# Kernel tuning notes

Hardware: AMD Instinct MI355X
Metric: run time of the kernel (lower is better)

Reference implementation:

```python
import jax, jax.numpy as jnp
import numpy as np

V = 32          # num_variables
T = 48          # num_time_bins
D = 512         # d_model
H = 8           # num_heads
HD = D // H     # head_dim = 64
OD = 16         # observation_dim
B = 4


def setup_inputs() -> dict:
    key = jax.random.key(0)
    ks = jax.random.split(key, 20)
    s = 0.02
    inp = {
        'h': jax.random.normal(ks[0], (B, T, V, D), jnp.float32),
        'observation_state': jax.random.normal(ks[1], (B, T, V, 2), jnp.float32),
        'Wq': jax.random.normal(ks[2], (D, D), jnp.float32) * s,
        'bq': jnp.zeros((D,), jnp.float32),
        'Wk': jax.random.normal(ks[3], (D, D), jnp.float32) * s,
        'bk': jnp.zeros((D,), jnp.float32),
        'Wv': jax.random.normal(ks[4], (D, D), jnp.float32) * s,
        'bv': jnp.zeros((D,), jnp.float32),
        'Wo': jax.random.normal(ks[5], (D, D), jnp.float32) * s,
        'bo': jnp.zeros((D,), jnp.float32),
        'Woq': jax.random.normal(ks[6], (2, H * OD), jnp.float32) * 0.5,
        'boq': jnp.zeros((H * OD,), jnp.float32),
        'Wok': jax.random.normal(ks[7], (2, H * OD), jnp.float32) * 0.5,
        'bok': jnp.zeros((H * OD,), jnp.float32),
        'variable_bias': jax.random.normal(ks[8], (H, V, V), jnp.float32) * 0.01,
        'relative_time_bias': jax.random.normal(ks[9], (H, 2 * T - 1), jnp.float32) * 0.01,
    }
    return inp


def reference(h, observation_state, Wq, bq, Wk, bk, Wv, bv, Wo, bo,
              Woq, boq, Wok, bok, variable_bias, relative_time_bias):
    N = T * V
    scale = 1.0 / np.sqrt(HD)
    obs_scale = 1.0 / np.sqrt(OD)

    # static index buffers (constants)
    flat_var_ids = jnp.tile(jnp.arange(V), T)                       # [N]
    flat_time_ids = jnp.repeat(jnp.arange(T), V)                    # [N]
    rel_index = flat_time_ids[:, None] - flat_time_ids[None, :] + (T - 1)  # [N,N]

    fh = h.reshape(B, N, D)
    fo = observation_state.reshape(B, N, 2)

    def heads(x, nh, hd):
        return x.reshape(B, N, nh, hd).transpose(0, 2, 1, 3)  # [B,H,N,hd]

    q = heads(fh @ Wq + bq, H, HD)
    k = heads(fh @ Wk + bk, H, HD)
    v = heads(fh @ Wv + bv, H, HD)
    oq = heads(fo @ Woq + boq, H, OD)
    ok = heads(fo @ Wok + bok, H, OD)

    content = jnp.einsum('bhnd,bhmd->bhnm', q, k) * scale
    obs = jnp.einsum('bhnd,bhmd->bhnm', oq, ok) * obs_scale
    var_scores = variable_bias[:, flat_var_ids[:, None], flat_var_ids[None, :]]  # [H,N,N]
    time_scores = relative_time_bias[:, rel_index]                                # [H,N,N]

    scores = content + obs + var_scores[None] + time_scores[None]
    attn = jax.nn.softmax(scores, axis=-1)  # dropout off (inference)
    out = jnp.einsum('bhnm,bhmd->bhnd', attn, v)
    out = out.transpose(0, 2, 1, 3).reshape(B, N, D)
    out = out @ Wo + bo
    return out.reshape(B, T, V, D)
```

## Files before the change

kernel.cpp:

```cpp
#include <hip/hip_runtime.h>
#include <math.h>

typedef __bf16 bf16x8 __attribute__((ext_vector_type(8)));
typedef float f32x4 __attribute__((ext_vector_type(4)));
typedef short short4v __attribute__((ext_vector_type(4)));

#define NB 4
#define NT 48
#define NV 32
#define ND 512
#define NH 8
#define NN 1536
#define NBN 6144
#define L2E 1.44269504f

#define GLOAD_LDS(g, l) \
    __builtin_amdgcn_global_load_lds( \
        (const __attribute__((address_space(1))) void*)(g), \
        (__attribute__((address_space(3))) void*)(l), 16, 0, 0)

__global__ __launch_bounds__(256) void prep(
    const float* __restrict__ h, const float* __restrict__ obs,
    const float* __restrict__ Wq, const float* __restrict__ Wk,
    const float* __restrict__ Wv, const float* __restrict__ Wo,
    const float* __restrict__ bq, const float* __restrict__ bk,
    const float* __restrict__ bv,
    const float* __restrict__ Wok, const float* __restrict__ bok,
    __bf16* __restrict__ h_bf, __bf16* __restrict__ WcatT,
    __bf16* __restrict__ WoT, float* __restrict__ biascat,
    __bf16* __restrict__ kx)
{
    __shared__ float ts[64][68];
    const int tid = threadIdx.x;
    const int bx = blockIdx.x;
    if (bx < 1536) {
        int t = bx * 256 + tid;
        const float4* src = (const float4*)h + (size_t)t * 2;
        float4 a = src[0], b = src[1];
        __bf16 r[8] = {(__bf16)a.x, (__bf16)a.y, (__bf16)a.z, (__bf16)a.w,
                       (__bf16)b.x, (__bf16)b.y, (__bf16)b.z, (__bf16)b.w};
        *(uint4*)(h_bf + (size_t)t * 8) = *(uint4*)r;
    } else if (bx < 1792) {
        int bw = bx - 1536;
        const int p = bw >> 6, tile = bw & 63;
        const int k0 = (tile >> 3) * 64, c0 = (tile & 7) * 64;
        const float* W = (p == 0) ? Wq : (p == 1) ? Wk : (p == 2) ? Wv : Wo;
        const float scale = (p == 0) ? 0.125f * L2E : 1.0f;
        #pragma unroll
        for (int i = 0; i < 4; i++) {
            int r = (tid >> 4) + i * 16;
            float4 v = *(const float4*)(W + (size_t)(k0 + r) * 512 + c0 + (tid & 15) * 4);
            *(float4*)&ts[r][(tid & 15) * 4] = v;
        }
        __syncthreads();
        __bf16 tmp[16];
        #pragma unroll
        for (int j = 0; j < 16; j++)
            tmp[j] = (__bf16)(ts[(tid & 3) * 16 + j][tid >> 2] * scale);
        int crow = c0 + (tid >> 2);
        __bf16* dst = (p < 3)
            ? WcatT + ((size_t)(p * 512 + crow)) * 512 + k0 + (tid & 3) * 16
            : WoT   + ((size_t)crow) * 512 + k0 + (tid & 3) * 16;
        *(uint4*)dst = *(uint4*)tmp;
        *(uint4*)(dst + 8) = *(uint4*)(tmp + 8);
        if (p < 3 && k0 == 0 && tid < 64) {
            const float* bb = (p == 0) ? bq : (p == 1) ? bk : bv;
            biascat[p * 512 + c0 + tid] = bb[c0 + tid] * scale;
        }
    } else {
        int t = (bx - 1792) * 256 + tid;
        int row = t >> 1, half = t & 1;
        int bh = row / NN, n = row - bh * NN;
        int mt = n >> 6, wv = (n >> 4) & 3, l16k = n & 15;
        __bf16* dst = kx + (((size_t)(bh * 24 + mt) * 4 + wv) * 3 + 2) * 512
                         + (half * 2) * 128 + l16k * 8;
        if (half == 0) {
            int hh = bh & 7;
            int b = bh >> 3;
            size_t bn = (size_t)b * NN + n;
            float o0 = obs[bn * 2], o1 = obs[bn * 2 + 1];
            int f = hh * 16;
            __bf16 tmp[16];
            #pragma unroll
            for (int j = 0; j < 16; j++)
                tmp[j] = (__bf16)(o0 * Wok[f + j] + o1 * Wok[128 + f + j] + bok[f + j]);
            *(uint4*)dst         = *(uint4*)tmp;
            *(uint4*)(dst + 128) = *(uint4*)(tmp + 8);
        } else {
            uint4 z = {0, 0, 0, 0};
            *(uint4*)dst         = z;
            *(uint4*)(dst + 128) = z;
        }
    }
}

template<int TM, bool BF16OUT>
__global__ __launch_bounds__(256) void gemm_mfma(
    const __bf16* __restrict__ A, const __bf16* __restrict__ Bt,
    const float* __restrict__ bias, float* __restrict__ Cf,
    __bf16* __restrict__ qarr, __bf16* __restrict__ kx,
    __bf16* __restrict__ vt)
{
    constexpr int MT = TM / 32;
    __shared__ __align__(16) char smem[34816];
    char* const As0 = smem;
    char* const As1 = smem + TM * 64;
    char* const Bs0 = smem + TM * 128;
    char* const Bs1 = smem + TM * 128 + 8192;
    const int tid = threadIdx.x;
    const int w = tid >> 6, lane = tid & 63;
    const int quad = lane >> 4, l16 = lane & 15;
    const int wm = w >> 1, wn = w & 1;
    const int n0 = blockIdx.x * 128, m0 = blockIdx.y * TM;

    const int sm = tid >> 2;
    const int sk = ((tid & 3) ^ ((sm >> 1) & 3)) * 8;
    const __bf16* aptr = A  + (size_t)(m0 + sm) * 512 + sk;
    const __bf16* bptr = Bt + (size_t)(n0 + sm) * 512 + sk;

    f32x4 zero4 = {0.f, 0.f, 0.f, 0.f};
    f32x4 acc[MT][4];
    #pragma unroll
    for (int i = 0; i < MT; i++)
        #pragma unroll
        for (int j = 0; j < 4; j++) acc[i][j] = zero4;

    auto STAGE = [&](char* dA, char* dB, int kt) {
        GLOAD_LDS(aptr + kt, dA + tid * 16);
        if (TM == 128) GLOAD_LDS(aptr + 64 * 512 + kt, dA + 4096 + tid * 16);
        GLOAD_LDS(bptr + kt, dB + tid * 16);
        GLOAD_LDS(bptr + 64 * 512 + kt, dB + 4096 + tid * 16);
    };
    auto COMPUTE = [&](const char* Asb, const char* Bsb) {
        bf16x8 af[MT], bfr[4];
        #pragma unroll
        for (int mt = 0; mt < MT; mt++) {
            int rr = wm * (TM / 2) + mt * 16 + l16;
            af[mt] = *(const bf16x8*)(Asb + rr * 64 + (quad ^ ((rr >> 1) & 3)) * 16);
        }
        #pragma unroll
        for (int nt = 0; nt < 4; nt++) {
            int rr = wn * 64 + nt * 16 + l16;
            bfr[nt] = *(const bf16x8*)(Bsb + rr * 64 + (quad ^ ((rr >> 1) & 3)) * 16);
        }
        #pragma unroll
        for (int mt = 0; mt < MT; mt++)
            #pragma unroll
            for (int nt = 0; nt < 4; nt++)
                acc[mt][nt] = __builtin_amdgcn_mfma_f32_16x16x32_bf16(
                    af[mt], bfr[nt], acc[mt][nt], 0, 0, 0);
    };

    STAGE(As0, Bs0, 0);
    asm volatile("s_waitcnt vmcnt(0)" ::: "memory");
    __builtin_amdgcn_s_barrier();
    for (int kt = 0; kt < 512; kt += 64) {
        STAGE(As1, Bs1, kt + 32);
        COMPUTE(As0, Bs0);
        asm volatile("s_waitcnt vmcnt(0)" ::: "memory");
        __builtin_amdgcn_s_barrier();
        if (kt + 64 < 512) STAGE(As0, Bs0, kt + 64);
        COMPUTE(As1, Bs1);
        asm volatile("s_waitcnt vmcnt(0)" ::: "memory");
        __builtin_amdgcn_s_barrier();
    }

    __syncthreads();
    if (BF16OUT) {
        if (n0 >= 1024) {
            __bf16* CsT = (__bf16*)smem;
            #pragma unroll
            for (int nt = 0; nt < 4; nt++) {
                int cl = wn * 64 + nt * 16 + l16;
                float bia = bias[n0 + cl];
                #pragma unroll
                for (int mt = 0; mt < MT; mt++) {
                    int rl0 = wm * (TM / 2) + mt * 16 + quad * 4;
                    __bf16 pk[4];
                    #pragma unroll
                    for (int r = 0; r < 4; r++)
                        pk[r] = (__bf16)(acc[mt][nt][r] + bia);
                    *(uint2*)&CsT[cl * 136 + rl0] = *(uint2*)pk;
                }
            }
            __syncthreads();
            int cl = tid >> 1, half = tid & 1;
            int f0 = (n0 + cl) & 511;
            int hh = f0 >> 6, d = f0 & 63;
            int dt = d >> 4, l16v = d & 15;
            int bidx = m0 / NN, nm = m0 - bidx * NN;
            int bh = bidx * 8 + hh;
            int mtv = (nm >> 6) + half;
            #pragma unroll
            for (int j = 0; j < 8; j++) {
                uint4 v = *(uint4*)&CsT[cl * 136 + half * 64 + j * 8];
                __bf16* pp = (__bf16*)&v;
                size_t fo = (((size_t)(bh * 24 + mtv) * 4 + (j >> 1)) * 4 + dt) * 256;
                int q0 = (j & 1) * 2;
                *(uint2*)(vt + fo + q0 * 64 + l16v * 4)       = *(uint2*)&pp[0];
                *(uint2*)(vt + fo + (q0 + 1) * 64 + l16v * 4) = *(uint2*)&pp[4];
            }
        } else {
            __bf16* Cs = (__bf16*)smem;
            #pragma unroll
            for (int mt = 0; mt < MT; mt++)
                #pragma unroll
                for (int nt = 0; nt < 4; nt++) {
                    int cl = wn * 64 + nt * 16 + l16;
                    float bia = bias[n0 + cl];
                    #pragma unroll
                    for (int r = 0; r < 4; r++) {
                        int rl = wm * (TM / 2) + mt * 16 + quad * 4 + r;
                        Cs[rl * 132 + cl] = (__bf16)(acc[mt][nt][r] + bia);
                    }
                }
            __syncthreads();
            int rl = tid >> 1, hb = tid & 1;
            int grow = m0 + rl;
            int col0 = n0 + hb * 64;
            int p = col0 >> 9, f0 = col0 & 511, hh = f0 >> 6;
            int bidx = grow / NN, n = grow - bidx * NN;
            if (p == 0) {
                __bf16* dst = qarr + (size_t)grow * 512 + f0;
                #pragma unroll
                for (int j = 0; j < 8; j++) {
                    uint2 lo = *(uint2*)&Cs[rl * 132 + hb * 64 + j * 8];
                    uint2 hi = *(uint2*)&Cs[rl * 132 + hb * 64 + j * 8 + 4];
                    uint4 v = {lo.x, lo.y, hi.x, hi.y};
                    *(uint4*)(dst + j * 8) = v;
                }
            } else {
                int mtk = n >> 6, wv = (n >> 4) & 3, l16k = n & 15;
                size_t fb = ((size_t)((bidx * 8 + hh) * 24 + mtk) * 4 + wv) * 1536;
                #pragma unroll
                for (int j = 0; j < 8; j++) {
                    uint2 lo = *(uint2*)&Cs[rl * 132 + hb * 64 + j * 8];
                    uint2 hi = *(uint2*)&Cs[rl * 132 + hb * 64 + j * 8 + 4];
                    uint4 v = {lo.x, lo.y, hi.x, hi.y};
                    *(uint4*)(kx + fb + (j >> 2) * 512 + (j & 3) * 128 + l16k * 8) = v;
                }
            }
        }
    } else {
        float* Csf = (float*)smem;
        #pragma unroll
        for (int mt = 0; mt < MT; mt++)
            #pragma unroll
            for (int nt = 0; nt < 4; nt++) {
                int cl = wn * 64 + nt * 16 + l16;
                float bia = bias[n0 + cl];
                #pragma unroll
                for (int r = 0; r < 4; r++) {
                    int rl = wm * (TM / 2) + mt * 16 + quad * 4 + r;
                    Csf[rl * 132 + cl] = acc[mt][nt][r] + bia;
                }
            }
        __syncthreads();
        int rl = tid >> 2, q4 = tid & 3;
        float* dst = Cf + (size_t)(m0 + rl) * 512 + n0 + q4 * 32;
        #pragma unroll
        for (int j = 0; j < 8; j++) {
            uint4 v = *(uint4*)&Csf[rl * 132 + q4 * 32 + j * 4];
            *(uint4*)(dst + j * 4) = v;
        }
    }
}

__global__ __launch_bounds__(256) void attn_mfma(
    const __bf16* __restrict__ qarr, const __bf16* __restrict__ kx,
    const __bf16* __restrict__ vt, const float* __restrict__ obs,
    const float* __restrict__ Woq, const float* __restrict__ boq,
    const float* __restrict__ varb, const float* __restrict__ rtb,
    __bf16* __restrict__ aout)
{
    __shared__ float Or[64][68];
    __shared__ float lps[4][64];
    __shared__ float2 rts2[96];

    const int tid = threadIdx.x;
    const int w = tid >> 6, lane = tid & 63;
    const int quad = lane >> 4, l16 = lane & 15;
    const int bh = blockIdx.x, qt = blockIdx.y;
    const int b = bh >> 3, h = bh & 7;
    const int n0 = qt * 64;

    if (tid < 95) {
        float a = rtb[h * 95 + tid] * L2E;
        float c = (tid < 94) ? rtb[h * 95 + tid + 1] * L2E : 0.f;
        rts2[tid].x = a;
        rts2[tid].y = c;
    }

    const __bf16* kwb = kx + ((size_t)bh * 24 * 4 + w) * 1536 + lane * 8;
    const __bf16* vwb = vt + ((size_t)bh * 24 * 4 + w) * 1024 + lane * 4;

    bf16x8 qf[4][3];
    #pragma unroll
    for (int nt = 0; nt < 4; nt++) {
        const size_t qrow = (size_t)(b * NN + n0 + nt * 16 + l16);
        qf[nt][0] = *(const bf16x8*)(qarr + qrow * 512 + h * 64 + quad * 8);
        qf[nt][1] = *(const bf16x8*)(qarr + qrow * 512 + h * 64 + 32 + quad * 8);
        uint4 a2u = {0u, 0u, 0u, 0u};
        if (quad < 2) {
            float o0 = obs[qrow * 2], o1 = obs[qrow * 2 + 1];
            int f = h * 16 + quad * 8;
            const float scq = 0.25f * L2E;
            __bf16 tmp[8];
            #pragma unroll
            for (int j = 0; j < 8; j++)
                tmp[j] = (__bf16)(scq * (o0 * Woq[f + j] + o1 * Woq[128 + f + j]
                                         + boq[f + j]));
            a2u = *(uint4*)tmp;
        }
        qf[nt][2] = *(bf16x8*)&a2u;
    }

    const float* vbp = varb + h * 1024 + (w & 1) * 16 + quad * 4;
    f32x4 vvA = *(const f32x4*)(vbp + l16 * 32);
    f32x4 vvB = *(const f32x4*)(vbp + (16 + l16) * 32);
    vvA *= L2E; vvB *= L2E;

    const int rbase = 2 * qt - (w >> 1) + 47;

    f32x4 zero4 = {0.f, 0.f, 0.f, 0.f};
    f32x4 o_p[4][4];
    #pragma unroll
    for (int i = 0; i < 4; i++)
        #pragma unroll
        for (int j = 0; j < 4; j++) o_p[i][j] = zero4;
    float lp_s[4] = {0.f, 0.f, 0.f, 0.f};

    bf16x8 kc[3]; short4v vc[4];
    #pragma unroll
    for (int ks = 0; ks < 3; ks++) kc[ks] = *(const bf16x8*)(kwb + ks * 512);
    #pragma unroll
    for (int dt = 0; dt < 4; dt++) vc[dt] = *(const short4v*)(vwb + dt * 256);

    __syncthreads();

    for (int mt = 0; mt < 24; mt++) {
        bf16x8 kn[3]; short4v vn[4];
        if (mt + 1 < 24) {
            const __bf16* kp = kwb + (size_t)(mt + 1) * 6144;
            const __bf16* vp = vwb + (size_t)(mt + 1) * 4096;
            #pragma unroll
            for (int ks = 0; ks < 3; ks++) kn[ks] = *(const bf16x8*)(kp + ks * 512);
            #pragma unroll
            for (int dt = 0; dt < 4; dt++) vn[dt] = *(const short4v*)(vp + dt * 256);
        }

        f32x4 sc[4];
        __builtin_amdgcn_s_setprio(1);
        #pragma unroll
        for (int nt = 0; nt < 4; nt++) {
            f32x4 d = zero4;
            #pragma unroll
            for (int ks = 0; ks < 3; ks++)
                d = __builtin_amdgcn_mfma_f32_16x16x32_bf16(kc[ks], qf[nt][ks], d, 0, 0, 0);
            sc[nt] = d;
        }
        __builtin_amdgcn_s_setprio(0);

        float2 tb = rts2[rbase - 2 * mt];
        short4v pf[4];
        #pragma unroll
        for (int nt = 0; nt < 4; nt++) {
            float tbx = (nt < 2) ? tb.x : tb.y;
            const f32x4& vv = (nt & 1) ? vvB : vvA;
            union { __bf16 e[4]; short4v s; } pk;
            #pragma unroll
            for (int r = 0; r < 4; r++) {
                float p = exp2f(sc[nt][r] + vv[r] + tbx);
                lp_s[nt] += p;
                pk.e[r] = (__bf16)p;
            }
            pf[nt] = pk.s;
        }

        __builtin_amdgcn_s_setprio(1);
        #pragma unroll
        for (int nt = 0; nt < 4; nt++)
            #pragma unroll
            for (int dt = 0; dt < 4; dt++)
                o_p[dt][nt] = __builtin_amdgcn_mfma_f32_16x16x16bf16_1k(
                    vc[dt], pf[nt], o_p[dt][nt], 0, 0, 0);
        __builtin_amdgcn_s_setprio(0);

        if (mt + 1 < 24) {
            #pragma unroll
            for (int ks = 0; ks < 3; ks++) kc[ks] = kn[ks];
            #pragma unroll
            for (int dt = 0; dt < 4; dt++) vc[dt] = vn[dt];
        }
    }

    #pragma unroll
    for (int nt = 0; nt < 4; nt++) {
        lp_s[nt] += __shfl_xor(lp_s[nt], 16);
        lp_s[nt] += __shfl_xor(lp_s[nt], 32);
    }
    if (quad == 0) {
        #pragma unroll
        for (int nt = 0; nt < 4; nt++) lps[w][nt * 16 + l16] = lp_s[nt];
    }

    #pragma unroll
    for (int ws = 0; ws < 4; ws++) {
        if (w == ws) {
            #pragma unroll
            for (int dt = 0; dt < 4; dt++)
                #pragma unroll
                for (int nt = 0; nt < 4; nt++) {
                    float* dst = &Or[nt * 16 + l16][dt * 16 + quad * 4];
                    if (ws == 0) *(f32x4*)dst = o_p[dt][nt];
                    else {
                        f32x4 t = *(f32x4*)dst;
                        *(f32x4*)dst = t + o_p[dt][nt];
                    }
                }
        }
        __syncthreads();
    }

    int n = tid >> 2, dq = tid & 3;
    float linv = 1.0f / (lps[0][n] + lps[1][n] + lps[2][n] + lps[3][n]);
    __bf16 ov[16];
    #pragma unroll
    for (int jj = 0; jj < 4; jj++) {
        f32x4 t = *(f32x4*)&Or[n][dq * 16 + jj * 4];
        ov[jj * 4 + 0] = (__bf16)(t[0] * linv);
        ov[jj * 4 + 1] = (__bf16)(t[1] * linv);
        ov[jj * 4 + 2] = (__bf16)(t[2] * linv);
        ov[jj * 4 + 3] = (__bf16)(t[3] * linv);
    }
    size_t abase = ((size_t)(b * NN) + n0 + n) * 512 + h * 64 + dq * 16;
    *(uint4*)(aout + abase)     = *(uint4*)&ov[0];
    *(uint4*)(aout + abase + 8) = *(uint4*)&ov[8];
}

extern "C" void kernel_launch(void* const* d_in, const int* in_sizes, int n_in,
                              void* d_out, int out_size, void* d_ws, size_t ws_size,
                              hipStream_t stream)
{
    const float* h_   = (const float*)d_in[0];
    const float* obs  = (const float*)d_in[1];
    const float* Wq   = (const float*)d_in[2];
    const float* bq   = (const float*)d_in[3];
    const float* Wk   = (const float*)d_in[4];
    const float* bk   = (const float*)d_in[5];
    const float* Wv   = (const float*)d_in[6];
    const float* bv   = (const float*)d_in[7];
    const float* Wo   = (const float*)d_in[8];
    const float* bo   = (const float*)d_in[9];
    const float* Woq  = (const float*)d_in[10];
    const float* boq  = (const float*)d_in[11];
    const float* Wok  = (const float*)d_in[12];
    const float* bok  = (const float*)d_in[13];
    const float* varb = (const float*)d_in[14];
    const float* rtb  = (const float*)d_in[15];
    float* out = (float*)d_out;

    char* ws = (char*)d_ws;
    __bf16* h_bf    = (__bf16*)ws;                 ws += (size_t)NBN * 512 * 2;
    __bf16* qarr    = (__bf16*)ws;                 ws += (size_t)NBN * 512 * 2;
    __bf16* vt      = (__bf16*)ws;                 ws += (size_t)NBN * 512 * 2;
    __bf16* kx      = (__bf16*)ws;                 ws += ((size_t)32 * NN * 96 + 64) * 2;
    __bf16* attnout = (__bf16*)ws;                 ws += (size_t)NBN * 512 * 2;
    __bf16* WcatT   = (__bf16*)ws;                 ws += (size_t)1536 * 512 * 2;
    __bf16* WoT     = (__bf16*)ws;                 ws += (size_t)512 * 512 * 2;
    float*  biascat = (float*)ws;                  ws += 1536 * 4;

    prep<<<dim3(2176), dim3(256), 0, stream>>>(
        h_, obs, Wq, Wk, Wv, Wo, bq, bk, bv, Wok, bok,
        h_bf, WcatT, WoT, biascat, kx);
    gemm_mfma<128, true><<<dim3(12, 48), dim3(256), 0, stream>>>(
        h_bf, WcatT, biascat, nullptr, qarr, kx, vt);
    attn_mfma<<<dim3(32, 24), dim3(256), 0, stream>>>(qarr, kx, vt, obs, Woq, boq,
                                                      varb, rtb, attnout);
    gemm_mfma<64, false><<<dim3(4, 96), dim3(256), 0, stream>>>(
        attnout, WoT, bo, out, nullptr, nullptr, nullptr);
}
```

Before: 186.3 us.

## Stage Q fragments in LDS, double-buffer K/V registers, compute row sums via MFMA

The Q fragments move out of registers into shared memory, where they alias the output-reduction buffer, and each wave reloads them from LDS per tile. This is meant to reduce VGPR pressure. K/V prefetch becomes an explicit two-slot ping-pong, so the per-iteration register copies go away. The softmax denominator is now accumulated with an MFMA against a vector of ones instead of scalar adds and shuffles. In exchange there is extra LDS traffic in the inner loop and an extra MFMA per tile, and the denominator now sums bf16-rounded probabilities.

```diff
diff --git a/kernel.cpp b/kernel.cpp
--- a/kernel.cpp
+++ b/kernel.cpp
@@ -273,9 +273,12 @@
     const float* __restrict__ varb, const float* __restrict__ rtb,
     __bf16* __restrict__ aout)
 {
-    __shared__ float Or[64][68];
+    __shared__ __align__(16) char smu[64 * 68 * 4];
     __shared__ float lps[4][64];
     __shared__ float2 rts2[96];
+
+    float (*Or)[68] = (float (*)[68])smu;
+    __bf16* Qs = (__bf16*)smu;
 
     const int tid = threadIdx.x;
     const int w = tid >> 6, lane = tid & 63;
@@ -284,6 +287,19 @@
     const int b = bh >> 3, h = bh & 7;
     const int n0 = qt * 64;
 
+    const __bf16* kwb = kx + ((size_t)bh * 24 * 4 + w) * 1536 + lane * 8;
+    const __bf16* vwb = vt + ((size_t)bh * 24 * 4 + w) * 1024 + lane * 4;
+
+    bf16x8 kA[3], kB[3]; short4v vA_[4], vB_[4];
+    #pragma unroll
+    for (int ks = 0; ks < 3; ks++) kA[ks] = *(const bf16x8*)(kwb + ks * 512);
+    #pragma unroll
+    for (int dt = 0; dt < 4; dt++) vA_[dt] = *(const short4v*)(vwb + dt * 256);
+    #pragma unroll
+    for (int ks = 0; ks < 3; ks++) kB[ks] = *(const bf16x8*)(kwb + 6144 + ks * 512);
+    #pragma unroll
+    for (int dt = 0; dt < 4; dt++) vB_[dt] = *(const short4v*)(vwb + 4096 + dt * 256);
+
     if (tid < 95) {
         float a = rtb[h * 95 + tid] * L2E;
         float c = (tid < 94) ? rtb[h * 95 + tid + 1] * L2E : 0.f;
@@ -291,15 +307,10 @@
         rts2[tid].y = c;
     }
 
-    const __bf16* kwb = kx + ((size_t)bh * 24 * 4 + w) * 1536 + lane * 8;
-    const __bf16* vwb = vt + ((size_t)bh * 24 * 4 + w) * 1024 + lane * 4;
-
-    bf16x8 qf[4][3];
-    #pragma unroll
-    for (int nt = 0; nt < 4; nt++) {
-        const size_t qrow = (size_t)(b * NN + n0 + nt * 16 + l16);
-        qf[nt][0] = *(const bf16x8*)(qarr + qrow * 512 + h * 64 + quad * 8);
-        qf[nt][1] = *(const bf16x8*)(qarr + qrow * 512 + h * 64 + 32 + quad * 8);
+    {
+        const size_t qrow = (size_t)(b * NN + n0 + w * 16 + l16);
+        bf16x8 f0 = *(const bf16x8*)(qarr + qrow * 512 + h * 64 + quad * 8);
+        bf16x8 f1 = *(const bf16x8*)(qarr + qrow * 512 + h * 64 + 32 + quad * 8);
         uint4 a2u = {0u, 0u, 0u, 0u};
         if (quad < 2) {
             float o0 = obs[qrow * 2], o1 = obs[qrow * 2 + 1];
@@ -312,7 +323,10 @@
                                          + boq[f + j]));
             a2u = *(uint4*)tmp;
         }
-        qf[nt][2] = *(bf16x8*)&a2u;
+        __bf16* qdst = Qs + ((size_t)(w * 3) * 64 + lane) * 8;
+        *(bf16x8*)(qdst)        = f0;
+        *(bf16x8*)(qdst + 512)  = f1;
+        *(bf16x8*)(qdst + 1024) = *(bf16x8*)&a2u;
     }
 
     const float* vbp = varb + h * 1024 + (w & 1) * 16 + quad * 4;
@@ -321,88 +335,80 @@
     vvA *= L2E; vvB *= L2E;
 
     const int rbase = 2 * qt - (w >> 1) + 47;
+    const __bf16* qsl = Qs + lane * 8;
+
+    union { __bf16 e[4]; short4v s; } one_u;
+    #pragma unroll
+    for (int j = 0; j < 4; j++) one_u.e[j] = (__bf16)1.0f;
+    const short4v ones = one_u.s;
 
     f32x4 zero4 = {0.f, 0.f, 0.f, 0.f};
     f32x4 o_p[4][4];
-    #pragma unroll
-    for (int i = 0; i < 4; i++)
+    f32x4 lpa[4];
+    #pragma unroll
+    for (int i = 0; i < 4; i++) {
+        lpa[i] = zero4;
         #pragma unroll
         for (int j = 0; j < 4; j++) o_p[i][j] = zero4;
-    float lp_s[4] = {0.f, 0.f, 0.f, 0.f};
-
-    bf16x8 kc[3]; short4v vc[4];
-    #pragma unroll
-    for (int ks = 0; ks < 3; ks++) kc[ks] = *(const bf16x8*)(kwb + ks * 512);
-    #pragma unroll
-    for (int dt = 0; dt < 4; dt++) vc[dt] = *(const short4v*)(vwb + dt * 256);
+    }
 
     __syncthreads();
 
-    for (int mt = 0; mt < 24; mt++) {
-        bf16x8 kn[3]; short4v vn[4];
-        if (mt + 1 < 24) {
-            const __bf16* kp = kwb + (size_t)(mt + 1) * 6144;
-            const __bf16* vp = vwb + (size_t)(mt + 1) * 4096;
-            #pragma unroll
-            for (int ks = 0; ks < 3; ks++) kn[ks] = *(const bf16x8*)(kp + ks * 512);
-            #pragma unroll
-            for (int dt = 0; dt < 4; dt++) vn[dt] = *(const short4v*)(vp + dt * 256);
-        }
-
-        f32x4 sc[4];
-        __builtin_amdgcn_s_setprio(1);
+    auto COMPUTE = [&](const bf16x8* kc, const short4v* vc, int mt) {
+        float2 tb = rts2[rbase - 2 * mt];
         #pragma unroll
         for (int nt = 0; nt < 4; nt++) {
+            bf16x8 q0 = *(const bf16x8*)(qsl + (nt * 3 + 0) * 512);
+            bf16x8 q1 = *(const bf16x8*)(qsl + (nt * 3 + 1) * 512);
+            bf16x8 q2 = *(const bf16x8*)(qsl + (nt * 3 + 2) * 512);
             f32x4 d = zero4;
-            #pragma unroll
-            for (int ks = 0; ks < 3; ks++)
-                d = __builtin_amdgcn_mfma_f32_16x16x32_bf16(kc[ks], qf[nt][ks], d, 0, 0, 0);
-            sc[nt] = d;
-        }
-        __builtin_amdgcn_s_setprio(0);
-
-        float2 tb = rts2[rbase - 2 * mt];
-        short4v pf[4];
-        #pragma unroll
-        for (int nt = 0; nt < 4; nt++) {
+            d = __builtin_amdgcn_mfma_f32_16x16x32_bf16(kc[0], q0, d, 0, 0, 0);
+            d = __builtin_amdgcn_mfma_f32_16x16x32_bf16(kc[1], q1, d, 0, 0, 0);
+            d = __builtin_amdgcn_mfma_f32_16x16x32_bf16(kc[2], q2, d, 0, 0, 0);
             float tbx = (nt < 2) ? tb.x : tb.y;
             const f32x4& vv = (nt & 1) ? vvB : vvA;
             union { __bf16 e[4]; short4v s; } pk;
             #pragma unroll
-            for (int r = 0; r < 4; r++) {
-                float p = exp2f(sc[nt][r] + vv[r] + tbx);
-                lp_s[nt] += p;
-                pk.e[r] = (__bf16)p;
-            }
-            pf[nt] = pk.s;
-        }
-
-        __builtin_amdgcn_s_setprio(1);
-        #pragma unroll
-        for (int nt = 0; nt < 4; nt++)
+            for (int r = 0; r < 4; r++)
+                pk.e[r] = (__bf16)exp2f(d[r] + vv[r] + tbx);
+            short4v pf = pk.s;
+            lpa[nt] = __builtin_amdgcn_mfma_f32_16x16x16bf16_1k(
+                ones, pf, lpa[nt], 0, 0, 0);
             #pragma unroll
             for (int dt = 0; dt < 4; dt++)
                 o_p[dt][nt] = __builtin_amdgcn_mfma_f32_16x16x16bf16_1k(
-                    vc[dt], pf[nt], o_p[dt][nt], 0, 0, 0);
-        __builtin_amdgcn_s_setprio(0);
-
-        if (mt + 1 < 24) {
-            #pragma unroll
-            for (int ks = 0; ks < 3; ks++) kc[ks] = kn[ks];
-            #pragma unroll
-            for (int dt = 0; dt < 4; dt++) vc[dt] = vn[dt];
-        }
-    }
-
-    #pragma unroll
-    for (int nt = 0; nt < 4; nt++) {
-        lp_s[nt] += __shfl_xor(lp_s[nt], 16);
-        lp_s[nt] += __shfl_xor(lp_s[nt], 32);
-    }
+                    vc[dt], pf, o_p[dt][nt], 0, 0, 0);
+        }
+    };
+
+    for (int i = 0; i < 11; i++) {
+        COMPUTE(kA, vA_, 2 * i);
+        {
+            const __bf16* kp = kwb + (size_t)(2 * i + 2) * 6144;
+            const __bf16* vp = vwb + (size_t)(2 * i + 2) * 4096;
+            #pragma unroll
+            for (int ks = 0; ks < 3; ks++) kA[ks] = *(const bf16x8*)(kp + ks * 512);
+            #pragma unroll
+            for (int dt = 0; dt < 4; dt++) vA_[dt] = *(const short4v*)(vp + dt * 256);
+        }
+        COMPUTE(kB, vB_, 2 * i + 1);
+        {
+            const __bf16* kp = kwb + (size_t)(2 * i + 3) * 6144;
+            const __bf16* vp = vwb + (size_t)(2 * i + 3) * 4096;
+            #pragma unroll
+            for (int ks = 0; ks < 3; ks++) kB[ks] = *(const bf16x8*)(kp + ks * 512);
+            #pragma unroll
+            for (int dt = 0; dt < 4; dt++) vB_[dt] = *(const short4v*)(vp + dt * 256);
+        }
+    }
+    COMPUTE(kA, vA_, 22);
+    COMPUTE(kB, vB_, 23);
+
     if (quad == 0) {
         #pragma unroll
-        for (int nt = 0; nt < 4; nt++) lps[w][nt * 16 + l16] = lp_s[nt];
-    }
+        for (int nt = 0; nt < 4; nt++) lps[w][nt * 16 + l16] = lpa[nt][0];
+    }
+    __syncthreads();
 
     #pragma unroll
     for (int ws = 0; ws < 4; ws++) {
```

After: 185.6 us. Within noise of the previous version (-0.4%).
